# Optimization experiments

Hardware: AMD Instinct MI355X
Metric: run time of the kernel (lower is better)

Reference implementation:

```python
import jax, jax.numpy as jnp
import numpy as np

T, B, N_INP, N_HID, N_OUT = 512, 128, 256, 1024, 128


def setup_inputs() -> dict:
    key = jax.random.key(0)
    ks = jax.random.split(key, 7)
    x = jax.random.normal(ks[0], (T, B, N_INP), dtype=jnp.float32)
    # PyTorch RNNCell/Linear default init: U(-1/sqrt(fan_in), 1/sqrt(fan_in))
    s_h = 1.0 / np.sqrt(N_HID)
    W_ih = jax.random.uniform(ks[1], (N_HID, N_INP), jnp.float32, -s_h, s_h)
    W_hh = jax.random.uniform(ks[2], (N_HID, N_HID), jnp.float32, -s_h, s_h)
    b_ih = jax.random.uniform(ks[3], (N_HID,), jnp.float32, -s_h, s_h)
    b_hh = jax.random.uniform(ks[4], (N_HID,), jnp.float32, -s_h, s_h)
    W_ro = jax.random.uniform(ks[5], (N_OUT, N_HID), jnp.float32, -s_h, s_h)
    b_ro = jax.random.uniform(ks[6], (N_OUT,), jnp.float32, -s_h, s_h)
    return {"x": x, "W_ih": W_ih, "W_hh": W_hh, "b_ih": b_ih,
            "b_hh": b_hh, "W_ro": W_ro, "b_ro": b_ro}


def reference(x, W_ih, W_hh, b_ih, b_hh, W_ro, b_ro):
    # x: [T, B, n_inp]; recurrence: state = tanh(x_t W_ih^T + b_ih + state W_hh^T + b_hh)
    batch = x.shape[1]
    n_hid = W_hh.shape[0]
    state0 = jnp.zeros((batch, n_hid), dtype=x.dtype)

    # Precompute the input projection for all timesteps in one big GEMM.
    x_proj = jnp.einsum('tbi,hi->tbh', x, W_ih) + b_ih + b_hh  # [T, B, n_hid]

    def step(state, xp_t):
        new_state = jnp.tanh(xp_t + state @ W_hh.T)
        return new_state, None

    final_state, _ = jax.lax.scan(step, state0, x_proj)
    # readout applied to final hidden state only (stateOnly=None path)
    return final_state @ W_ro.T + b_ro  # [B, n_out]
```

## Files before the change

### kernel.cpp

```cpp
#include <hip/hip_runtime.h>
#include <hip/hip_bf16.h>
#include <stdint.h>


#define TSTEPS 512
#define BATCH  128
#define NI     256
#define NH     1024
#define NO     128
#define NBLK   128
#define NTHR   512
#define NWAVE  8
#define BG     16
#define COLS   64

typedef __attribute__((ext_vector_type(8))) short s16x8;
typedef __attribute__((ext_vector_type(4))) float f32x4;
typedef __attribute__((ext_vector_type(4))) unsigned u32x4;
typedef unsigned long long ull;

__device__ __forceinline__ unsigned short f2bf_rne(float f) {
  unsigned u = __builtin_bit_cast(unsigned, f);
  unsigned r = u + 0x7fffu + ((u >> 16) & 1u);
  return (unsigned short)(r >> 16);
}
__device__ __forceinline__ float bf2f(unsigned short h) {
  unsigned u = ((unsigned)h) << 16;
  return __builtin_bit_cast(float, u);
}
__device__ __forceinline__ void split_bf(float v, short &hi, short &lo) {
  unsigned short h = f2bf_rne(v);
  hi = (short)h;
  lo = (short)f2bf_rne(v - bf2f(h));
}
__device__ __forceinline__ f32x4 mfma16(s16x8 a, s16x8 b, f32x4 c) {
  return __builtin_amdgcn_mfma_f32_16x16x32_bf16(a, b, c, 0, 0, 0);
}
__device__ __forceinline__ float fast_tanh(float a) {
  float cl = fminf(fmaxf(a, -15.f), 15.f);
  float e  = __expf(2.f * cl);
  return (e - 1.f) / (e + 1.f);
}

#define SIDX(g, w, r, k) ((((size_t)(g) * NWAVE + (w)) * BG + (r)) * 128 + (k))

__global__ __launch_bounds__(NTHR, 2)
void rnn_persistent(const float* __restrict__ x,
                    const float* __restrict__ W_ih,
                    const float* __restrict__ W_hh,
                    const float* __restrict__ b_ih,
                    const float* __restrict__ b_hh,
                    unsigned*    __restrict__ SP)
{
  const int tid  = threadIdx.x;
  const int wave = tid >> 6;
  const int lane = tid & 63;
  const int lr   = lane & 15;
  const int lq   = lane >> 4;
  const int g    = blockIdx.x & 7;
  const int m    = blockIdx.x >> 3;
  const int row0 = g * BG;
  const int h0   = m * COLS;
  const int kq0  = wave * 128;
  const int iq0  = wave * 32;

  __shared__ float red[2][NWAVE][1024];

  s16x8 whh_hi[4][4], whh_lo[4][4];
  #pragma unroll
  for (int nt = 0; nt < 4; ++nt) {
    const int h = h0 + nt * 16 + lr;
    #pragma unroll
    for (int kb = 0; kb < 4; ++kb) {
      const float* p = W_hh + (size_t)h * NH + kq0 + kb * 32 + lq * 8;
      s16x8 hi, lo;
      #pragma unroll
      for (int j = 0; j < 8; ++j) { short a, b; split_bf(p[j], a, b); hi[j] = a; lo[j] = b; }
      whh_hi[nt][kb] = hi; whh_lo[nt][kb] = lo;
    }
  }
  s16x8 wih_hi[4], wih_lo[4];
  #pragma unroll
  for (int nt = 0; nt < 4; ++nt) {
    const int h = h0 + nt * 16 + lr;
    const float* p = W_ih + (size_t)h * NI + iq0 + lq * 8;
    s16x8 hi, lo;
    #pragma unroll
    for (int j = 0; j < 8; ++j) { short a, b; split_bf(p[j], a, b); hi[j] = a; lo[j] = b; }
    wih_hi[nt] = hi; wih_lo[nt] = lo;
  }

  const int er = tid >> 5;
  const int ec = (tid & 31) * 2;
  const float bias0 = b_ih[h0 + ec]     + b_hh[h0 + ec];
  const float bias1 = b_ih[h0 + ec + 1] + b_hh[h0 + ec + 1];
  const int wsl = m >> 1;
  const int klo = (m & 1) * 64 + ec;

  unsigned* buf0 = SP;
  unsigned* buf1 = SP + (size_t)BATCH * NH;

  float xf[8];
  {
    const float* xp = x + (size_t)(row0 + lr) * NI + iq0 + lq * 8;
    #pragma unroll
    for (int j = 0; j < 8; ++j) xf[j] = xp[j];
  }

  const unsigned* sb0 = buf0 + SIDX(g, wave, lr, lq * 8);
  const unsigned* sb1 = buf1 + SIDX(g, wave, lr, lq * 8);

  for (int t = 0; t < TSTEPS; ++t) {
    f32x4 acc[4];
    #pragma unroll
    for (int nt = 0; nt < 4; ++nt) acc[nt] = (f32x4){0.f, 0.f, 0.f, 0.f};
    {
      s16x8 xhi, xlo;
      #pragma unroll
      for (int j = 0; j < 8; ++j) { short a, b; split_bf(xf[j], a, b); xhi[j] = a; xlo[j] = b; }
      #pragma unroll
      for (int nt = 0; nt < 4; ++nt) {
        acc[nt] = mfma16(xhi, wih_hi[nt], acc[nt]);
        acc[nt] = mfma16(xhi, wih_lo[nt], acc[nt]);
        acc[nt] = mfma16(xlo, wih_hi[nt], acc[nt]);
      }
    }
    const unsigned etag = (unsigned)((t >> 1) & 1);
    const unsigned* sb = (t & 1) ? sb1 : sb0;
    u32x4 sv0, sv1, sv2, sv3, sv4, sv5, sv6, sv7;
    {
      const u32x4 e4 = (u32x4){etag, etag, etag, etag};
      bool use_ic = false;
      for (;;) {
        if (use_ic) {
          asm volatile(
            "global_load_dwordx4 %0, %8, off sc1\n\t"
            "global_load_dwordx4 %1, %8, off offset:16 sc1\n\t"
            "global_load_dwordx4 %2, %8, off offset:128 sc1\n\t"
            "global_load_dwordx4 %3, %8, off offset:144 sc1\n\t"
            "global_load_dwordx4 %4, %8, off offset:256 sc1\n\t"
            "global_load_dwordx4 %5, %8, off offset:272 sc1\n\t"
            "global_load_dwordx4 %6, %8, off offset:384 sc1\n\t"
            "global_load_dwordx4 %7, %8, off offset:400 sc1\n\t"
            "s_waitcnt vmcnt(0)"
            : "=&v"(sv0), "=&v"(sv1), "=&v"(sv2), "=&v"(sv3),
              "=&v"(sv4), "=&v"(sv5), "=&v"(sv6), "=&v"(sv7)
            : "v"(sb) : "memory");
        } else {
          asm volatile(
            "global_load_dwordx4 %0, %8, off sc0\n\t"
            "global_load_dwordx4 %1, %8, off offset:16 sc0\n\t"
            "global_load_dwordx4 %2, %8, off offset:128 sc0\n\t"
            "global_load_dwordx4 %3, %8, off offset:144 sc0\n\t"
            "global_load_dwordx4 %4, %8, off offset:256 sc0\n\t"
            "global_load_dwordx4 %5, %8, off offset:272 sc0\n\t"
            "global_load_dwordx4 %6, %8, off offset:384 sc0\n\t"
            "global_load_dwordx4 %7, %8, off offset:400 sc0\n\t"
            "s_waitcnt vmcnt(0)"
            : "=&v"(sv0), "=&v"(sv1), "=&v"(sv2), "=&v"(sv3),
              "=&v"(sv4), "=&v"(sv5), "=&v"(sv6), "=&v"(sv7)
            : "v"(sb) : "memory");
        }
        u32x4 b4 = (sv0 ^ e4) | (sv1 ^ e4) | (sv2 ^ e4) | (sv3 ^ e4)
                 | (sv4 ^ e4) | (sv5 ^ e4) | (sv6 ^ e4) | (sv7 ^ e4);
        unsigned bad = b4[0] | b4[1] | b4[2] | b4[3];
        if ((bad & 1u) == 0) break;
        use_ic = !use_ic;
      }
    }
    {
      const int tn = (t + 1 < TSTEPS) ? (t + 1) : t;
      const float* xp = x + (size_t)tn * BATCH * NI + (size_t)(row0 + lr) * NI + iq0 + lq * 8;
      #pragma unroll
      for (int j = 0; j < 8; ++j) xf[j] = xp[j];
    }
    {
      unsigned sw[32];
      #pragma unroll
      for (int e = 0; e < 4; ++e) {
        sw[0  + e] = sv0[e]; sw[4  + e] = sv1[e];
        sw[8  + e] = sv2[e]; sw[12 + e] = sv3[e];
        sw[16 + e] = sv4[e]; sw[20 + e] = sv5[e];
        sw[24 + e] = sv6[e]; sw[28 + e] = sv7[e];
      }
      #pragma unroll
      for (int kb = 0; kb < 4; ++kb) {
        s16x8 shi, slo;
        #pragma unroll
        for (int j = 0; j < 8; ++j) {
          unsigned w = sw[kb * 8 + j];
          shi[j] = (short)(w >> 16);
          slo[j] = (short)(w & 0xffffu);
        }
        #pragma unroll
        for (int nt = 0; nt < 4; ++nt) {
          acc[nt] = mfma16(shi, whh_hi[nt][kb], acc[nt]);
          acc[nt] = mfma16(shi, whh_lo[nt][kb], acc[nt]);
          acc[nt] = mfma16(slo, whh_hi[nt][kb], acc[nt]);
        }
      }
    }
    const int rbi = t & 1;
    #pragma unroll
    for (int nt = 0; nt < 4; ++nt)
      #pragma unroll
      for (int r = 0; r < 4; ++r)
        red[rbi][wave][(lq * 4 + r) * 64 + nt * 16 + lr] = acc[nt][r];
    __syncthreads();
    {
      float s0 = bias0, s1 = bias1;
      #pragma unroll
      for (int w = 0; w < NWAVE; ++w) {
        float2 v = *(const float2*)&red[rbi][w][er * 64 + ec];
        s0 += v.x; s1 += v.y;
      }
      float t0 = fast_tanh(s0), t1 = fast_tanh(s1);
      const unsigned otag = (unsigned)(((t + 1) >> 1) & 1);
      unsigned short h0b = f2bf_rne(t0);
      unsigned       l0b = ((f2bf_rne(t0 - bf2f(h0b)) & 0xfffeu) | otag);
      unsigned short h1b = f2bf_rne(t1);
      unsigned       l1b = ((f2bf_rne(t1 - bf2f(h1b)) & 0xfffeu) | otag);
      ull pk = ((ull)(((unsigned)h1b << 16) | l1b) << 32)
             |  (ull)(((unsigned)h0b << 16) | l0b);
      ull* op = (ull*)(((t + 1) & 1 ? buf1 : buf0) + SIDX(g, wsl, er, klo));
      __hip_atomic_store(op, pk, __ATOMIC_RELAXED, __HIP_MEMORY_SCOPE_AGENT);
    }
  }
}

__global__ __launch_bounds__(256)
void init_buf1(unsigned* __restrict__ SP) {
  const int i = blockIdx.x * 256 + threadIdx.x;
  SP[BATCH * NH + i] = 1u;
}

__global__ __launch_bounds__(512)
void rnn_readout(const unsigned* __restrict__ SP,
                 const float* __restrict__ W_ro,
                 const float* __restrict__ b_ro,
                 float* __restrict__ out)
{
  __shared__ float srow[4][NH];
  const int b0 = blockIdx.x * 4;
  for (int i = threadIdx.x; i < 4 * NH; i += 512) {
    const int b = b0 + (i >> 10);
    const int h = i & 1023;
    unsigned u = SP[SIDX(b >> 4, h >> 7, b & 15, h & 127)];
    srow[i >> 10][h] = bf2f((unsigned short)(u >> 16)) + bf2f((unsigned short)(u & 0xffffu));
  }
  __syncthreads();
  const int bb = threadIdx.x >> 7;
  const int o  = threadIdx.x & 127;
  const float* wr = W_ro + (size_t)o * NH;
  float s = 0.f;
  #pragma unroll 4
  for (int k = 0; k < NH; ++k) s += srow[bb][k] * wr[k];
  out[(size_t)(b0 + bb) * NO + o] = s + b_ro[o];
}

extern "C" void kernel_launch(void* const* d_in, const int* in_sizes, int n_in,
                              void* d_out, int out_size, void* d_ws, size_t ws_size,
                              hipStream_t stream) {
  (void)in_sizes; (void)n_in; (void)out_size; (void)ws_size;
  const float* x    = (const float*)d_in[0];
  const float* W_ih = (const float*)d_in[1];
  const float* W_hh = (const float*)d_in[2];
  const float* b_ih = (const float*)d_in[3];
  const float* b_hh = (const float*)d_in[4];
  const float* W_ro = (const float*)d_in[5];
  const float* b_ro = (const float*)d_in[6];
  float* out = (float*)d_out;

  unsigned* SP = (unsigned*)d_ws;

  hipMemsetAsync(SP, 0, (size_t)BATCH * NH * sizeof(unsigned), stream);
  init_buf1<<<(BATCH * NH) / 256, 256, 0, stream>>>(SP);

  rnn_persistent<<<NBLK, NTHR, 0, stream>>>(x, W_ih, W_hh, b_ih, b_hh, SP);
  rnn_readout<<<BATCH / 4, 512, 0, stream>>>(SP, W_ro, b_ro, out);
}
```

Baseline: 1.837 ms.

## Mirror hidden state into a second buffer to speed cross-block polling

Each step's hidden-state store now goes to two buffers: a plain store to the local buffer and an sc1 store to a mirror copy. Consumers poll the local buffer with sc0 loads and fall back to the mirror with sc1 loads only on every eighth miss, instead of alternating cache policies on every retry. The intent is to cut the latency of the inter-block handoff while still guaranteeing progress when a stale line stays in cache. The cost is double the store traffic, four state buffers in the workspace, and a readout that reads from the mirror.

```diff
diff --git a/kernel.cpp b/kernel.cpp
--- a/kernel.cpp
+++ b/kernel.cpp
@@ -13,6 +13,7 @@
 #define NWAVE  8
 #define BG     16
 #define COLS   64
+#define SPBUF  ((size_t)BATCH * NH)
 
 typedef __attribute__((ext_vector_type(8))) short s16x8;
 typedef __attribute__((ext_vector_type(4))) float f32x4;
@@ -97,8 +98,10 @@
   const int wsl = m >> 1;
   const int klo = (m & 1) * 64 + ec;
 
-  unsigned* buf0 = SP;
-  unsigned* buf1 = SP + (size_t)BATCH * NH;
+  unsigned* lb0 = SP;
+  unsigned* lb1 = SP + SPBUF;
+  unsigned* mr0 = SP + 2 * SPBUF;
+  unsigned* mr1 = SP + 3 * SPBUF;
 
   float xf[8];
   {
@@ -107,8 +110,10 @@
     for (int j = 0; j < 8; ++j) xf[j] = xp[j];
   }
 
-  const unsigned* sb0 = buf0 + SIDX(g, wave, lr, lq * 8);
-  const unsigned* sb1 = buf1 + SIDX(g, wave, lr, lq * 8);
+  const size_t soff = SIDX(g, wave, lr, lq * 8);
+  const unsigned* sbL[2] = { lb0 + soff, lb1 + soff };
+  const unsigned* sbM[2] = { mr0 + soff, mr1 + soff };
+  const size_t poff = SIDX(g, wsl, er, klo);
 
   for (int t = 0; t < TSTEPS; ++t) {
     f32x4 acc[4];
@@ -126,13 +131,33 @@
       }
     }
     const unsigned etag = (unsigned)((t >> 1) & 1);
-    const unsigned* sb = (t & 1) ? sb1 : sb0;
+    const unsigned* sb = sbL[t & 1];
+    const unsigned* mb = sbM[t & 1];
     u32x4 sv0, sv1, sv2, sv3, sv4, sv5, sv6, sv7;
     {
       const u32x4 e4 = (u32x4){etag, etag, etag, etag};
-      bool use_ic = false;
+      int miss = 0;
       for (;;) {
-        if (use_ic) {
+        asm volatile(
+          "global_load_dwordx4 %0, %8, off sc0\n\t"
+          "global_load_dwordx4 %1, %8, off offset:16 sc0\n\t"
+          "global_load_dwordx4 %2, %8, off offset:128 sc0\n\t"
+          "global_load_dwordx4 %3, %8, off offset:144 sc0\n\t"
+          "global_load_dwordx4 %4, %8, off offset:256 sc0\n\t"
+          "global_load_dwordx4 %5, %8, off offset:272 sc0\n\t"
+          "global_load_dwordx4 %6, %8, off offset:384 sc0\n\t"
+          "global_load_dwordx4 %7, %8, off offset:400 sc0\n\t"
+          "s_waitcnt vmcnt(0)"
+          : "=&v"(sv0), "=&v"(sv1), "=&v"(sv2), "=&v"(sv3),
+            "=&v"(sv4), "=&v"(sv5), "=&v"(sv6), "=&v"(sv7)
+          : "v"(sb) : "memory");
+        {
+          u32x4 b4 = (sv0 ^ e4) | (sv1 ^ e4) | (sv2 ^ e4) | (sv3 ^ e4)
+                   | (sv4 ^ e4) | (sv5 ^ e4) | (sv6 ^ e4) | (sv7 ^ e4);
+          unsigned bad = b4[0] | b4[1] | b4[2] | b4[3];
+          if ((bad & 1u) == 0) break;
+        }
+        if (((++miss) & 7) == 0) {
           asm volatile(
             "global_load_dwordx4 %0, %8, off sc1\n\t"
             "global_load_dwordx4 %1, %8, off offset:16 sc1\n\t"
@@ -145,27 +170,12 @@
             "s_waitcnt vmcnt(0)"
             : "=&v"(sv0), "=&v"(sv1), "=&v"(sv2), "=&v"(sv3),
               "=&v"(sv4), "=&v"(sv5), "=&v"(sv6), "=&v"(sv7)
-            : "v"(sb) : "memory");
-        } else {
-          asm volatile(
-            "global_load_dwordx4 %0, %8, off sc0\n\t"
-            "global_load_dwordx4 %1, %8, off offset:16 sc0\n\t"
-            "global_load_dwordx4 %2, %8, off offset:128 sc0\n\t"
-            "global_load_dwordx4 %3, %8, off offset:144 sc0\n\t"
-            "global_load_dwordx4 %4, %8, off offset:256 sc0\n\t"
-            "global_load_dwordx4 %5, %8, off offset:272 sc0\n\t"
-            "global_load_dwordx4 %6, %8, off offset:384 sc0\n\t"
-            "global_load_dwordx4 %7, %8, off offset:400 sc0\n\t"
-            "s_waitcnt vmcnt(0)"
-            : "=&v"(sv0), "=&v"(sv1), "=&v"(sv2), "=&v"(sv3),
-              "=&v"(sv4), "=&v"(sv5), "=&v"(sv6), "=&v"(sv7)
-            : "v"(sb) : "memory");
-        }
-        u32x4 b4 = (sv0 ^ e4) | (sv1 ^ e4) | (sv2 ^ e4) | (sv3 ^ e4)
-                 | (sv4 ^ e4) | (sv5 ^ e4) | (sv6 ^ e4) | (sv7 ^ e4);
-        unsigned bad = b4[0] | b4[1] | b4[2] | b4[3];
-        if ((bad & 1u) == 0) break;
-        use_ic = !use_ic;
+            : "v"(mb) : "memory");
+          u32x4 b4 = (sv0 ^ e4) | (sv1 ^ e4) | (sv2 ^ e4) | (sv3 ^ e4)
+                   | (sv4 ^ e4) | (sv5 ^ e4) | (sv6 ^ e4) | (sv7 ^ e4);
+          unsigned bad = b4[0] | b4[1] | b4[2] | b4[3];
+          if ((bad & 1u) == 0) break;
+        }
       }
     }
     {
@@ -222,16 +232,20 @@
       unsigned       l1b = ((f2bf_rne(t1 - bf2f(h1b)) & 0xfffeu) | otag);
       ull pk = ((ull)(((unsigned)h1b << 16) | l1b) << 32)
              |  (ull)(((unsigned)h0b << 16) | l0b);
-      ull* op = (ull*)(((t + 1) & 1 ? buf1 : buf0) + SIDX(g, wsl, er, klo));
-      __hip_atomic_store(op, pk, __ATOMIC_RELAXED, __HIP_MEMORY_SCOPE_AGENT);
+      unsigned* lbd = ((t + 1) & 1) ? lb1 : lb0;
+      unsigned* mrd = ((t + 1) & 1) ? mr1 : mr0;
+      ull* opL = (ull*)(lbd + poff);
+      ull* opM = (ull*)(mrd + poff);
+      asm volatile("global_store_dwordx2 %0, %1, off" :: "v"(opL), "v"(pk) : "memory");
+      asm volatile("global_store_dwordx2 %0, %1, off sc1" :: "v"(opM), "v"(pk) : "memory");
     }
   }
 }
 
 __global__ __launch_bounds__(256)
-void init_buf1(unsigned* __restrict__ SP) {
-  const int i = blockIdx.x * 256 + threadIdx.x;
-  SP[BATCH * NH + i] = 1u;
+void init_sp(unsigned* __restrict__ SP) {
+  const size_t i = (size_t)blockIdx.x * 256 + threadIdx.x;
+  SP[i] = (unsigned)((i >> 17) & 1);
 }
 
 __global__ __launch_bounds__(512)
@@ -241,11 +255,12 @@
                  float* __restrict__ out)
 {
   __shared__ float srow[4][NH];
+  const unsigned* MIR0 = SP + 2 * SPBUF;
   const int b0 = blockIdx.x * 4;
   for (int i = threadIdx.x; i < 4 * NH; i += 512) {
     const int b = b0 + (i >> 10);
     const int h = i & 1023;
-    unsigned u = SP[SIDX(b >> 4, h >> 7, b & 15, h & 127)];
+    unsigned u = MIR0[SIDX(b >> 4, h >> 7, b & 15, h & 127)];
     srow[i >> 10][h] = bf2f((unsigned short)(u >> 16)) + bf2f((unsigned short)(u & 0xffffu));
   }
   __syncthreads();
@@ -273,8 +288,7 @@
 
   unsigned* SP = (unsigned*)d_ws;
 
-  hipMemsetAsync(SP, 0, (size_t)BATCH * NH * sizeof(unsigned), stream);
-  init_buf1<<<(BATCH * NH) / 256, 256, 0, stream>>>(SP);
+  init_sp<<<(4 * BATCH * NH) / 256, 256, 0, stream>>>(SP);
 
   rnn_persistent<<<NBLK, NTHR, 0, stream>>>(x, W_ih, W_hh, b_ih, b_hh, SP);
   rnn_readout<<<BATCH / 4, 512, 0, stream>>>(SP, W_ro, b_ro, out);
```

Measured after the change: 2.127 ms. +15.8%, slower.
